# Kernel tuning notes

Hardware: AMD Instinct MI355X
Metric: run time of the kernel (lower is better)

Reference implementation:

```python
import jax, jax.numpy as jnp
import numpy as np

# Config (matches init_kwargs)
V = 32000      # vocab_size
H = 1024       # hidden_size
NH = 16        # num_heads
NKV = 4        # num_kv_heads
L = 4          # num_layers
FF = 4096      # intermediate_size
MAXPOS = 2048
HD = H // NH   # head_dim = 64
KVD = H * NKV // NH  # kv projection dim = 256
EPS = 1e-5


def setup_inputs() -> dict:
    key = jax.random.key(0)
    ks = iter(jax.random.split(key, 64))
    B, T = 1, 2048
    std = 0.02

    def w(shape):
        return jax.random.normal(next(ks), shape, dtype=jnp.float32) * std

    inp = {
        "input_ids": jax.random.randint(next(ks), (B, T), 0, V),
        "attention_mask": jnp.zeros((B, T), dtype=jnp.float32),
        "tok_emb": w((V, H)),
        "pos_emb": w((MAXPOS, H)),
        # stacked per-layer params; Linear weights stored as [in, out]
        "qW": w((L, H, H)),   "qb": jnp.zeros((L, H)),
        "kW": w((L, H, KVD)), "kb": jnp.zeros((L, KVD)),
        "vW": w((L, H, KVD)), "vb": jnp.zeros((L, KVD)),
        "oW": w((L, H, H)),   "ob": jnp.zeros((L, H)),
        "m1W": w((L, H, FF)), "m1b": jnp.zeros((L, FF)),
        "m2W": w((L, FF, H)), "m2b": jnp.zeros((L, H)),
        "ln1g": jnp.ones((L, H)), "ln1b": jnp.zeros((L, H)),
        "ln2g": jnp.ones((L, H)), "ln2b": jnp.zeros((L, H)),
        "lnfg": jnp.ones((H,)),   "lnfb": jnp.zeros((H,)),
        "headW": w((H, V)),  # head: Linear(H, V, bias=False), stored [in,out]
    }
    return inp


def _layer_norm(x, g, b):
    m = jnp.mean(x, axis=-1, keepdims=True)
    v = jnp.mean(jnp.square(x - m), axis=-1, keepdims=True)
    return (x - m) * jax.lax.rsqrt(v + EPS) * g + b


def _gqa_attn(x, mask, qW, qb, kW, kb, vW, vb, oW, ob):
    B, T, _ = x.shape
    G = NH // NKV  # query groups per kv head
    q = (x @ qW + qb).reshape(B, T, NH, HD).transpose(0, 2, 1, 3)        # [B,NH,T,HD]
    q = q.reshape(B, NKV, G, T, HD)                                      # [B,NKV,G,T,HD]
    k = (x @ kW + kb).reshape(B, T, NKV, HD).transpose(0, 2, 1, 3)       # [B,NKV,T,HD]
    v = (x @ vW + vb).reshape(B, T, NKV, HD).transpose(0, 2, 1, 3)       # [B,NKV,T,HD]
    # naive full score tensor [B,NKV,G,T,T] (as in the original module)
    scores = jnp.einsum("bkgqd,bksd->bkgqs", q, k) / jnp.sqrt(jnp.float32(HD))
    scores = scores + mask[:, None, None, None, :]  # additive mask over keys
    attn = jax.nn.softmax(scores, axis=-1)
    out = jnp.einsum("bkgqs,bksd->bkgqd", attn, v)                       # [B,NKV,G,T,HD]
    out = out.reshape(B, NH, T, HD).transpose(0, 2, 1, 3).reshape(B, T, H)
    return out @ oW + ob


def reference(input_ids, attention_mask, tok_emb, pos_emb,
              qW, qb, kW, kb, vW, vb, oW, ob,
              m1W, m1b, m2W, m2b,
              ln1g, ln1b, ln2g, ln2b, lnfg, lnfb, headW):
    B, T = input_ids.shape
    x = tok_emb[input_ids] + pos_emb[jnp.arange(T)][None, :, :]  # [B,T,H]
    for i in range(L):
        h = _layer_norm(x, ln1g[i], ln1b[i])
        x = x + _gqa_attn(h, attention_mask, qW[i], qb[i], kW[i], kb[i],
                          vW[i], vb[i], oW[i], ob[i])
        h = _layer_norm(x, ln2g[i], ln2b[i])
        h = jax.nn.gelu(h @ m1W[i] + m1b[i], approximate=False) @ m2W[i] + m2b[i]
        x = x + h
    x = _layer_norm(x, lnfg, lnfb)
    logits = x @ headW  # [B,T,V]
    return logits
```

## Files before the change

kernel.cpp:

```cpp
#include <hip/hip_runtime.h>
#include <stdint.h>
#include <math.h>

typedef __attribute__((ext_vector_type(8))) short bf16x8;
typedef __attribute__((ext_vector_type(4))) short bf16x4;
typedef __attribute__((ext_vector_type(4))) float f32x4;

__device__ __forceinline__ short f2bf(float f) {
  unsigned u = __builtin_bit_cast(unsigned, f);
  unsigned r = u + 0x7fffu + ((u >> 16) & 1u);
  return (short)(r >> 16);
}

__device__ __forceinline__ f32x4 mfma16(bf16x8 a, bf16x8 b, f32x4 c) {
  return __builtin_amdgcn_mfma_f32_16x16x32_bf16(a, b, c, 0, 0, 0);
}

__device__ __forceinline__ void gload16(const void* g, void* l) {
  __builtin_amdgcn_global_load_lds((const __attribute__((address_space(1))) void*)g,
                                   (__attribute__((address_space(3))) void*)l, 16, 0, 0);
}

__device__ __forceinline__ int swz(int row, int col) {
  return row * 64 + (((col >> 3) ^ (row & 7)) << 3) + (col & 7);
}

__global__ __launch_bounds__(256) void embed_k(const int* __restrict__ ids,
                                               const float* __restrict__ tok,
                                               const float* __restrict__ pos,
                                               float* __restrict__ x) {
  const int t = threadIdx.x, w = t >> 6, lane = t & 63;
  const int row = blockIdx.x * 4 + w;
  const int id = ids[row];
#pragma unroll
  for (int i = 0; i < 4; ++i) {
    const int c = (i * 64 + lane) * 4;
    const float4 a = *reinterpret_cast<const float4*>(tok + (size_t)id * 1024 + c);
    const float4 b = *reinterpret_cast<const float4*>(pos + (size_t)row * 1024 + c);
    float4 o = make_float4(a.x + b.x, a.y + b.y, a.z + b.z, a.w + b.w);
    *reinterpret_cast<float4*>(x + (size_t)row * 1024 + c) = o;
  }
}

__global__ __launch_bounds__(256) void ln_k(const float* __restrict__ x,
                                            const float* __restrict__ gw,
                                            const float* __restrict__ bw,
                                            short* __restrict__ out) {
  const int t = threadIdx.x, w = t >> 6, lane = t & 63;
  const int row = blockIdx.x * 4 + w;
  float4 v[4];
  float s = 0.f, q = 0.f;
#pragma unroll
  for (int i = 0; i < 4; ++i) {
    v[i] = *reinterpret_cast<const float4*>(x + (size_t)row * 1024 + (i * 64 + lane) * 4);
    s += v[i].x + v[i].y + v[i].z + v[i].w;
    q += v[i].x * v[i].x + v[i].y * v[i].y + v[i].z * v[i].z + v[i].w * v[i].w;
  }
#pragma unroll
  for (int o = 32; o > 0; o >>= 1) { s += __shfl_xor(s, o); q += __shfl_xor(q, o); }
  const float mean = s * (1.f / 1024.f);
  const float var  = q * (1.f / 1024.f) - mean * mean;
  const float rstd = rsqrtf(var + 1e-5f);
#pragma unroll
  for (int i = 0; i < 4; ++i) {
    const int c = (i * 64 + lane) * 4;
    const float4 gv = *reinterpret_cast<const float4*>(gw + c);
    const float4 bv = *reinterpret_cast<const float4*>(bw + c);
    bf16x4 ov = { f2bf((v[i].x - mean) * rstd * gv.x + bv.x),
                  f2bf((v[i].y - mean) * rstd * gv.y + bv.y),
                  f2bf((v[i].z - mean) * rstd * gv.z + bv.z),
                  f2bf((v[i].w - mean) * rstd * gv.w + bv.w) };
    *reinterpret_cast<bf16x4*>(out + (size_t)row * 1024 + c) = ov;
  }
}

__global__ __launch_bounds__(256) void tcvt_k(const float* __restrict__ W,
                                              short* __restrict__ Wt,
                                              int N, size_t inStride, size_t outStride,
                                              int rowOff, int ldOut, float scale) {
  __shared__ float T[128][68];
  const float* Win = W + blockIdx.z * inStride;
  short* Wout = Wt + blockIdx.z * outStride;
  const int n0 = blockIdx.x * 64, k0 = blockIdx.y * 128;
  const int t = threadIdx.x;
  const int nc = (t & 15) * 4, kr = t >> 4;
#pragma unroll
  for (int p = 0; p < 8; ++p) {
    const float4 v = *reinterpret_cast<const float4*>(Win + (size_t)(k0 + kr + 16 * p) * N + n0 + nc);
    T[kr + 16 * p][nc + 0] = v.x;
    T[kr + 16 * p][nc + 1] = v.y;
    T[kr + 16 * p][nc + 2] = v.z;
    T[kr + 16 * p][nc + 3] = v.w;
  }
  __syncthreads();
  const int n = t >> 2, ks = (t & 3) * 32;
  short tmp[32];
#pragma unroll
  for (int i = 0; i < 32; ++i) tmp[i] = f2bf(T[ks + i][n] * scale);
  short* op = Wout + (size_t)(rowOff + n0 + n) * ldOut + k0 + ks;
#pragma unroll
  for (int c = 0; c < 4; ++c)
    *reinterpret_cast<bf16x8*>(op + c * 8) = *reinterpret_cast<bf16x8*>(tmp + c * 8);
}

__global__ __launch_bounds__(256) void bqkv_k(const float* __restrict__ qb,
                                              const float* __restrict__ kb,
                                              const float* __restrict__ vb,
                                              float* __restrict__ o) {
  int l = blockIdx.y;
  int c = blockIdx.x * 256 + threadIdx.x;
  float v;
  if (c < 1024) v = qb[l * 1024 + c] * 0.125f;
  else if (c < 1280) v = kb[l * 256 + c - 1024];
  else v = vb[l * 256 + c - 1280];
  o[l * 1536 + c] = v;
}

__global__ __launch_bounds__(256) void vtr_k(const short* __restrict__ v, int vld,
                                             short* __restrict__ vt) {
  __shared__ short T[64][80];
  const int kvh = blockIdx.y;
  const int s0 = blockIdx.x * 64;
  const int t = threadIdx.x;
  const int row = t >> 3, ch = t & 7;
#pragma unroll
  for (int p = 0; p < 2; ++p) {
    int s = row + 32 * p;
    bf16x8 vv = *reinterpret_cast<const bf16x8*>(v + (size_t)(s0 + s) * vld + kvh * 64 + ch * 8);
    *reinterpret_cast<bf16x8*>(&T[s][ch * 8]) = vv;
  }
  __syncthreads();
#pragma unroll
  for (int p = 0; p < 2; ++p) {
    int d = row + 32 * p;
    short tmp[8];
#pragma unroll
    for (int i = 0; i < 8; ++i) tmp[i] = T[ch * 8 + i][d];
    *reinterpret_cast<bf16x8*>(vt + (size_t)(kvh * 64 + d) * 2048 + s0 + ch * 8) =
        *reinterpret_cast<bf16x8*>(tmp);
  }
}

template <int EPI, int XSWZ, int TILE>
__global__ __launch_bounds__(256, 4)
void gemm_bt(const short* __restrict__ A, const short* __restrict__ Wt,
             const float* __restrict__ bias, const float* __restrict__ resid,
             void* __restrict__ out, int M, int N, int K, int nbOff,
             short* __restrict__ vt) {
  constexpr int BN   = (TILE == 0) ? 128 : 64;
  constexpr int WN   = (TILE == 0) ? 64 : 32;
  constexpr int NT   = (TILE == 0) ? 4 : 2;
  constexpr int BISS = (TILE == 0) ? 4 : 2;
  __shared__ short As[128 * 64];
  __shared__ short Bs[BN * 64];
  const int t = threadIdx.x;
  const int lane = t & 63, w = t >> 6;
  const int g = lane >> 4, r = lane & 15;
  const int wr = w >> 1, wc = w & 1;

  int bx = blockIdx.x, by = blockIdx.y;
  if (XSWZ == 1) {
    const int nbx = gridDim.x, nby = gridDim.y, nwg = nbx * nby;
    const int bid = by * nbx + bx;
    const int q = nwg >> 3, rr = nwg & 7;
    const int xcd = bid & 7, loc = bid >> 3;
    const int sw = (xcd < rr ? xcd * (q + 1) : rr * (q + 1) + (xcd - rr) * q) + loc;
    by = sw % nby; bx = sw / nby;
  }
  const int m0 = by * 128, n0 = (bx + nbOff) * BN;

  f32x4 acc[4][NT];
#pragma unroll
  for (int i = 0; i < 4; ++i)
#pragma unroll
    for (int j = 0; j < NT; ++j) { f32x4 z = {0.f, 0.f, 0.f, 0.f}; acc[i][j] = z; }

  const int srow = lane >> 3, sslot = lane & 7;

  for (int k0 = 0; k0 < K; k0 += 64) {
#pragma unroll
    for (int i = 0; i < 4; ++i) {
      const int rowA = w * 32 + i * 8 + srow;
      const int colA = (sslot ^ (srow & 7)) << 3;
      gload16(A + (size_t)(m0 + rowA) * K + k0 + colA, &As[(w * 32 + i * 8) * 64]);
    }
#pragma unroll
    for (int i = 0; i < BISS; ++i) {
      const int rowB = w * (8 * BISS) + i * 8 + srow;
      const int colB = (sslot ^ (srow & 7)) << 3;
      gload16(Wt + (size_t)(n0 + rowB) * K + k0 + colB, &Bs[(w * (8 * BISS) + i * 8) * 64]);
    }
    __syncthreads();
#pragma unroll
    for (int kk = 0; kk < 64; kk += 32) {
      bf16x8 af[4], bfg[NT];
#pragma unroll
      for (int mt = 0; mt < 4; ++mt)
        af[mt] = *reinterpret_cast<const bf16x8*>(&As[swz(wr * 64 + mt * 16 + r, kk + g * 8)]);
#pragma unroll
      for (int nt = 0; nt < NT; ++nt)
        bfg[nt] = *reinterpret_cast<const bf16x8*>(&Bs[swz(wc * WN + nt * 16 + r, kk + g * 8)]);
#pragma unroll
      for (int mt = 0; mt < 4; ++mt)
#pragma unroll
        for (int nt = 0; nt < NT; ++nt)
          acc[mt][nt] = mfma16(af[mt], bfg[nt], acc[mt][nt]);
    }
    __syncthreads();
  }
#pragma unroll
  for (int nt = 0; nt < NT; ++nt) {
    const int col = n0 + wc * WN + nt * 16 + r;
    const float bv = (EPI == 3) ? 0.f : bias[col];
#pragma unroll
    for (int mt = 0; mt < 4; ++mt) {
      const int rowb = m0 + wr * 64 + mt * 16 + 4 * g;
      short vs[4];
#pragma unroll
      for (int j = 0; j < 4; ++j) {
        const int row = rowb + j;
        const size_t oi = (size_t)row * N + col;
        float vv = acc[mt][nt][j] + bv;
        if (EPI == 0) {
          ((short*)out)[oi] = f2bf(vv);
        } else if (EPI == 1) {
          vv = 0.5f * vv * (1.f + erff(vv * 0.70710678118654752f));
          ((short*)out)[oi] = f2bf(vv);
        } else if (EPI == 2) {
          ((float*)out)[oi] = resid[oi] + vv;
        } else if (EPI == 3) {
          ((float*)out)[oi] = vv;
        } else {
          short bb = f2bf(vv);
          ((short*)out)[oi] = bb;
          vs[j] = bb;
        }
      }
      if (EPI == 4 && col >= 1280) {
        bf16x4 pk = { vs[0], vs[1], vs[2], vs[3] };
        *reinterpret_cast<bf16x4*>(vt + (size_t)(col - 1280) * 2048 + rowb) = pk;
      }
    }
  }
}

template <int EPI>
__global__ __launch_bounds__(256)
void gemm_k(const short* __restrict__ A, const float* __restrict__ W,
            const float* __restrict__ bias, const float* resid, void* out,
            int M, int N, int K, float scale) {
  __shared__ short As[128 * 64];
  __shared__ short Bs[128 * 64];
  const int t = threadIdx.x;
  const int lane = t & 63;
  const int g = lane >> 4, r = lane & 15;
  const int wid = t >> 6, wr = wid >> 1, wc = wid & 1;
  const int m0 = blockIdx.y * 128, n0 = blockIdx.x * 128;
  f32x4 acc[4][4];
#pragma unroll
  for (int i = 0; i < 4; ++i)
#pragma unroll
    for (int j = 0; j < 4; ++j) { f32x4 z = {0.f, 0.f, 0.f, 0.f}; acc[i][j] = z; }
  const int arow = t >> 3, ac = t & 7;
  const int bnn = t >> 1, bkh = t & 1;
  for (int k0 = 0; k0 < K; k0 += 64) {
#pragma unroll
    for (int p = 0; p < 4; ++p) {
      int row = arow + 32 * p;
      bf16x8 av = *reinterpret_cast<const bf16x8*>(A + (size_t)(m0 + row) * K + k0 + ac * 8);
      *reinterpret_cast<bf16x8*>(&As[swz(row, ac * 8)]) = av;
    }
#pragma unroll
    for (int p = 0; p < 8; ++p) {
      int kg = 4 * (bkh + 2 * p);
      const float* wp = W + (size_t)(k0 + kg) * N + n0 + bnn;
      bf16x4 wv = { f2bf(wp[0]), f2bf(wp[(size_t)N]), f2bf(wp[(size_t)2 * N]), f2bf(wp[(size_t)3 * N]) };
      *reinterpret_cast<bf16x4*>(&Bs[swz(bnn, kg)]) = wv;
    }
    __syncthreads();
#pragma unroll
    for (int kk = 0; kk < 64; kk += 32) {
      bf16x8 af[4], bfg[4];
#pragma unroll
      for (int mt = 0; mt < 4; ++mt)
        af[mt] = *reinterpret_cast<const bf16x8*>(&As[swz(wr * 64 + mt * 16 + r, kk + g * 8)]);
#pragma unroll
      for (int nt = 0; nt < 4; ++nt)
        bfg[nt] = *reinterpret_cast<const bf16x8*>(&Bs[swz(wc * 64 + nt * 16 + r, kk + g * 8)]);
#pragma unroll
      for (int mt = 0; mt < 4; ++mt)
#pragma unroll
        for (int nt = 0; nt < 4; ++nt)
          acc[mt][nt] = mfma16(af[mt], bfg[nt], acc[mt][nt]);
    }
    __syncthreads();
  }
#pragma unroll
  for (int nt = 0; nt < 4; ++nt) {
    const int col = n0 + wc * 64 + nt * 16 + r;
    const float bv = (EPI == 3) ? 0.f : bias[col];
#pragma unroll
    for (int mt = 0; mt < 4; ++mt) {
#pragma unroll
      for (int j = 0; j < 4; ++j) {
        const int row = m0 + wr * 64 + mt * 16 + 4 * g + j;
        const size_t oi = (size_t)row * N + col;
        float vv = acc[mt][nt][j] + bv;
        if (EPI == 0) {
          ((short*)out)[oi] = f2bf(vv * scale);
        } else if (EPI == 1) {
          vv = 0.5f * vv * (1.f + erff(vv * 0.70710678118654752f));
          ((short*)out)[oi] = f2bf(vv);
        } else if (EPI == 2) {
          ((float*)out)[oi] = resid[oi] + vv;
        } else {
          ((float*)out)[oi] = vv;
        }
      }
    }
  }
}

__global__ __launch_bounds__(256) void attn_k(const short* __restrict__ q, int qld,
                                              const short* __restrict__ k, int kld,
                                              const short* __restrict__ vt,
                                              const float* __restrict__ mask,
                                              short* __restrict__ o) {
  __shared__ short Ks[2][64 * 64];
  __shared__ short Vs[2][64 * 64];
  const int t = threadIdx.x, lane = t & 63, w = t >> 6;
  const int g = lane >> 4, r = lane & 15;
  const int h = blockIdx.y, qb = blockIdx.x, kvh = h >> 2;
  const int qrow = qb * 64 + w * 16 + r;

  const short* qp = q + (size_t)qrow * qld + h * 64;
  bf16x8 qf0 = *reinterpret_cast<const bf16x8*>(qp + g * 8);
  bf16x8 qf1 = *reinterpret_cast<const bf16x8*>(qp + 32 + g * 8);

  const short* kbase = k + kvh * 64;
  const short* vbase = vt + (size_t)kvh * 64 * 2048;

  f32x4 oacc[4];
#pragma unroll
  for (int i = 0; i < 4; ++i) { f32x4 z = {0.f, 0.f, 0.f, 0.f}; oacc[i] = z; }
  float m_run = -INFINITY, l_run = 0.f;

  const int srow = w * 8 + (lane >> 3), schunk = lane & 7;

#pragma unroll
  for (int p = 0; p < 2; ++p) {
    const int rr = srow + 32 * p;
    const int cc = (schunk ^ (rr & 7)) << 3;
    gload16(kbase + (size_t)rr * kld + cc, (char*)Ks + p * 4096 + w * 1024);
    gload16(vbase + (size_t)rr * 2048 + cc, (char*)Vs + p * 4096 + w * 1024);
  }
  asm volatile("s_waitcnt vmcnt(0)" ::: "memory");
  __syncthreads();

  for (int it = 0; it < 32; ++it) {
    const int cur = it & 1;
    if (it < 31) {
      const int s1 = (it + 1) * 64;
#pragma unroll
      for (int p = 0; p < 2; ++p) {
        const int rr = srow + 32 * p;
        const int cc = (schunk ^ (rr & 7)) << 3;
        gload16(kbase + (size_t)(s1 + rr) * kld + cc,
                (char*)Ks + (cur ^ 1) * 8192 + p * 4096 + w * 1024);
        gload16(vbase + (size_t)rr * 2048 + s1 + cc,
                (char*)Vs + (cur ^ 1) * 8192 + p * 4096 + w * 1024);
      }
    }
    const int s0 = it * 64;
    const short* Kc = Ks[cur];
    const short* Vc = Vs[cur];

    f32x4 sa[4];
#pragma unroll
    for (int st = 0; st < 4; ++st) {
      bf16x8 kf0 = *reinterpret_cast<const bf16x8*>(&Kc[swz(st * 16 + r, g * 8)]);
      bf16x8 kf1 = *reinterpret_cast<const bf16x8*>(&Kc[swz(st * 16 + r, 32 + g * 8)]);
      f32x4 z = {0.f, 0.f, 0.f, 0.f};
      z = mfma16(kf0, qf0, z);
      z = mfma16(kf1, qf1, z);
      sa[st] = z;
    }
    float sv[16];
    float pmax = -INFINITY;
#pragma unroll
    for (int st = 0; st < 4; ++st) {
      const float4 mv = *reinterpret_cast<const float4*>(mask + s0 + st * 16 + 4 * g);
#pragma unroll
      for (int j = 0; j < 4; ++j) {
        float xx = sa[st][j] + ((const float*)&mv)[j];
        sv[st * 4 + j] = xx;
        pmax = fmaxf(pmax, xx);
      }
    }
    pmax = fmaxf(pmax, __shfl_xor(pmax, 16));
    pmax = fmaxf(pmax, __shfl_xor(pmax, 32));
    float m_new = fmaxf(m_run, pmax);
    float corr = __expf(m_run - m_new);
    float psum = 0.f;
    short pb[16];
#pragma unroll
    for (int i = 0; i < 16; ++i) {
      float p = __expf(sv[i] - m_new);
      psum += p;
      pb[i] = f2bf(p);
    }
    psum += __shfl_xor(psum, 16);
    psum += __shfl_xor(psum, 32);
    l_run = l_run * corr + psum;
    m_run = m_new;
#pragma unroll
    for (int dt = 0; dt < 4; ++dt)
#pragma unroll
      for (int j = 0; j < 4; ++j) oacc[dt][j] *= corr;

#pragma unroll
    for (int hs = 0; hs < 2; ++hs) {
      bf16x8 pf = { pb[hs * 8 + 0], pb[hs * 8 + 1], pb[hs * 8 + 2], pb[hs * 8 + 3],
                    pb[hs * 8 + 4], pb[hs * 8 + 5], pb[hs * 8 + 6], pb[hs * 8 + 7] };
#pragma unroll
      for (int dt = 0; dt < 4; ++dt) {
        int d = dt * 16 + r;
        int c1 = 4 * g + 32 * hs;
        bf16x4 va  = *reinterpret_cast<const bf16x4*>(&Vc[swz(d, c1)]);
        bf16x4 vb2 = *reinterpret_cast<const bf16x4*>(&Vc[swz(d, c1 + 16)]);
        bf16x8 vf = { va[0], va[1], va[2], va[3], vb2[0], vb2[1], vb2[2], vb2[3] };
        oacc[dt] = mfma16(vf, pf, oacc[dt]);
      }
    }
    asm volatile("s_waitcnt vmcnt(0)" ::: "memory");
    __syncthreads();
  }
  float inv = 1.f / l_run;
#pragma unroll
  for (int dt = 0; dt < 4; ++dt) {
    bf16x4 ov = { f2bf(oacc[dt][0] * inv), f2bf(oacc[dt][1] * inv),
                  f2bf(oacc[dt][2] * inv), f2bf(oacc[dt][3] * inv) };
    *reinterpret_cast<bf16x4*>(o + (size_t)qrow * 1024 + h * 64 + dt * 16 + 4 * g) = ov;
  }
}

extern "C" void kernel_launch(void* const* d_in, const int* in_sizes, int n_in,
                              void* d_out, int out_size, void* d_ws, size_t ws_size,
                              hipStream_t stream) {
  const int*   ids   = (const int*)d_in[0];
  const float* mask  = (const float*)d_in[1];
  const float* tok   = (const float*)d_in[2];
  const float* pos   = (const float*)d_in[3];
  const float* qW    = (const float*)d_in[4];
  const float* qbias = (const float*)d_in[5];
  const float* kW    = (const float*)d_in[6];
  const float* kbias = (const float*)d_in[7];
  const float* vW    = (const float*)d_in[8];
  const float* vbias = (const float*)d_in[9];
  const float* oW    = (const float*)d_in[10];
  const float* obias = (const float*)d_in[11];
  const float* m1W   = (const float*)d_in[12];
  const float* m1b   = (const float*)d_in[13];
  const float* m2W   = (const float*)d_in[14];
  const float* m2b   = (const float*)d_in[15];
  const float* ln1g  = (const float*)d_in[16];
  const float* ln1b  = (const float*)d_in[17];
  const float* ln2g  = (const float*)d_in[18];
  const float* ln2b  = (const float*)d_in[19];
  const float* lnfg  = (const float*)d_in[20];
  const float* lnfb  = (const float*)d_in[21];
  const float* headW = (const float*)d_in[22];
  float* out = (float*)d_out;

  char* ws = (char*)d_ws;
  float* x   = (float*)ws;
  short* xb  = (short*)(ws + 8388608ull);

  const size_t OFF_QKV  = 12582912ull;
  const size_t OFF_AO   = 18874368ull;
  const size_t OFF_FF   = 23068672ull;
  const size_t OFF_BQ   = 39845888ull;
  const size_t OFF_WQKV = 39870464ull;
  const size_t OFF_WO   = 52453376ull;
  const size_t OFF_WM1  = 60841984ull;
  const size_t OFF_WM2  = 94396416ull;
  const size_t OFF_WH   = 127950848ull;
  const size_t NEED     = 193486848ull;

  if (ws_size >= NEED) {
    short* qkv  = (short*)(ws + OFF_QKV);
    short* ao   = (short*)(ws + OFF_AO);
    short* ff   = (short*)(ws + OFF_FF);
    short* vt   = ff;
    float* bqv  = (float*)(ws + OFF_BQ);
    short* Wqkv = (short*)(ws + OFF_WQKV);
    short* Wo   = (short*)(ws + OFF_WO);
    short* Wm1  = (short*)(ws + OFF_WM1);
    short* Wm2  = (short*)(ws + OFF_WM2);
    short* Wh   = (short*)(ws + OFF_WH);

    tcvt_k<<<dim3(16, 8, 4), 256, 0, stream>>>(qW, Wqkv, 1024, 1048576ull, 1572864ull, 0, 1024, 0.125f);
    tcvt_k<<<dim3(4, 8, 4),  256, 0, stream>>>(kW, Wqkv, 256,  262144ull,  1572864ull, 1024, 1024, 1.f);
    tcvt_k<<<dim3(4, 8, 4),  256, 0, stream>>>(vW, Wqkv, 256,  262144ull,  1572864ull, 1280, 1024, 1.f);
    tcvt_k<<<dim3(16, 8, 4), 256, 0, stream>>>(oW, Wo, 1024, 1048576ull, 1048576ull, 0, 1024, 1.f);
    tcvt_k<<<dim3(64, 8, 4), 256, 0, stream>>>(m1W, Wm1, 4096, 4194304ull, 4194304ull, 0, 1024, 1.f);
    tcvt_k<<<dim3(16, 32, 4), 256, 0, stream>>>(m2W, Wm2, 1024, 4194304ull, 4194304ull, 0, 4096, 1.f);
    tcvt_k<<<dim3(500, 8, 1), 256, 0, stream>>>(headW, Wh, 32000, 0ull, 0ull, 0, 1024, 1.f);
    bqkv_k<<<dim3(6, 4), 256, 0, stream>>>(qbias, kbias, vbias, bqv);

    embed_k<<<512, 256, 0, stream>>>(ids, tok, pos, x);

    for (int l = 0; l < 4; ++l) {
      short* Wq_l  = Wqkv + (size_t)l * 1536 * 1024;
      short* Wo_l  = Wo   + (size_t)l * 1024 * 1024;
      short* Wm1_l = Wm1  + (size_t)l * 4096 * 1024;
      short* Wm2_l = Wm2  + (size_t)l * 1024 * 4096;

      ln_k<<<512, 256, 0, stream>>>(x, ln1g + l * 1024, ln1b + l * 1024, xb);
      gemm_bt<4, 0, 1><<<dim3(24, 16), 256, 0, stream>>>(xb, Wq_l, bqv + l * 1536, nullptr,
                                                         qkv, 2048, 1536, 1024, 0, vt);
      attn_k<<<dim3(32, 16), 256, 0, stream>>>(qkv, 1536, qkv + 1024, 1536, vt, mask, ao);
      gemm_bt<2, 0, 1><<<dim3(16, 16), 256, 0, stream>>>(ao, Wo_l, obias + l * 1024, x,
                                                         x, 2048, 1024, 1024, 0, nullptr);
      ln_k<<<512, 256, 0, stream>>>(x, ln2g + l * 1024, ln2b + l * 1024, xb);
      gemm_bt<1, 1, 1><<<dim3(64, 16), 256, 0, stream>>>(xb, Wm1_l, m1b + l * 4096, nullptr,
                                                         ff, 2048, 4096, 1024, 0, nullptr);
      gemm_bt<2, 1, 1><<<dim3(16, 16), 256, 0, stream>>>(ff, Wm2_l, m2b + l * 1024, x,
                                                         x, 2048, 1024, 4096, 0, nullptr);
    }
    ln_k<<<512, 256, 0, stream>>>(x, lnfg, lnfb, xb);
    gemm_bt<3, 1, 0><<<dim3(125, 16), 256, 0, stream>>>(xb, Wh, nullptr, nullptr,
                                                        out, 2048, 32000, 1024, 0, nullptr);
    gemm_bt<3, 1, 0><<<dim3(125, 16), 256, 0, stream>>>(xb, Wh, nullptr, nullptr,
                                                        out, 2048, 32000, 1024, 125, nullptr);
  } else {
    short* qbf = (short*)(ws + (12u << 20));
    short* kbf = (short*)(ws + (16u << 20));
    short* vbf = (short*)(ws + (17u << 20));
    short* ao  = (short*)(ws + (18u << 20));
    short* ff  = (short*)(ws + (22u << 20));
    short* vtf = (short*)(ws + (38u << 20));

    embed_k<<<512, 256, 0, stream>>>(ids, tok, pos, x);
    for (int l = 0; l < 4; ++l) {
      ln_k<<<512, 256, 0, stream>>>(x, ln1g + l * 1024, ln1b + l * 1024, xb);
      gemm_k<0><<<dim3(8, 16), 256, 0, stream>>>(xb, qW + (size_t)l * 1024 * 1024,
          qbias + l * 1024, nullptr, qbf, 2048, 1024, 1024, 0.125f);
      gemm_k<0><<<dim3(2, 16), 256, 0, stream>>>(xb, kW + (size_t)l * 1024 * 256,
          kbias + l * 256, nullptr, kbf, 2048, 256, 1024, 1.f);
      gemm_k<0><<<dim3(2, 16), 256, 0, stream>>>(xb, vW + (size_t)l * 1024 * 256,
          vbias + l * 256, nullptr, vbf, 2048, 256, 1024, 1.f);
      vtr_k<<<dim3(32, 4), 256, 0, stream>>>(vbf, 256, vtf);
      attn_k<<<dim3(32, 16), 256, 0, stream>>>(qbf, 1024, kbf, 256, vtf, mask, ao);
      gemm_k<2><<<dim3(8, 16), 256, 0, stream>>>(ao, oW + (size_t)l * 1024 * 1024,
          obias + l * 1024, x, x, 2048, 1024, 1024, 1.f);
      ln_k<<<512, 256, 0, stream>>>(x, ln2g + l * 1024, ln2b + l * 1024, xb);
      gemm_k<1><<<dim3(32, 16), 256, 0, stream>>>(xb, m1W + (size_t)l * 1024 * 4096,
          m1b + l * 4096, nullptr, ff, 2048, 4096, 1024, 1.f);
      gemm_k<2><<<dim3(8, 16), 256, 0, stream>>>(ff, m2W + (size_t)l * 4096 * 1024,
          m2b + l * 1024, x, x, 2048, 1024, 4096, 1.f);
    }
    ln_k<<<512, 256, 0, stream>>>(x, lnfg, lnfb, xb);
    gemm_k<3><<<dim3(250, 16), 256, 0, stream>>>(xb, headW, nullptr, nullptr, out,
        2048, 32000, 1024, 1.f);
  }
}
```

Baseline: 1.176 ms.

## Add 256x256 double-buffered LM-head GEMM kernel with XCD-aware block remap

```diff
diff --git a/kernel.cpp b/kernel.cpp
--- a/kernel.cpp
+++ b/kernel.cpp
@@ -138,6 +138,112 @@
     for (int i = 0; i < 8; ++i) tmp[i] = T[ch * 8 + i][d];
     *reinterpret_cast<bf16x8*>(vt + (size_t)(kvh * 64 + d) * 2048 + s0 + ch * 8) =
         *reinterpret_cast<bf16x8*>(tmp);
+  }
+}
+
+__global__ __launch_bounds__(512, 2)
+void gemm_h8(const short* __restrict__ A, const short* __restrict__ Wt,
+             float* __restrict__ out, int M, int N, int K) {
+  __shared__ short As[2][256 * 64];
+  __shared__ short Bs[2][256 * 64];
+  const int t = threadIdx.x;
+  const int lane = t & 63, w = t >> 6;
+  const int g = lane >> 4, r = lane & 15;
+  const int wm = w >> 2, wn = w & 3;
+
+  int bx = blockIdx.x, by = blockIdx.y;
+  {
+    const int nbx = gridDim.x, nby = gridDim.y, nwg = nbx * nby;
+    const int bid = by * nbx + bx;
+    const int q = nwg >> 3, rr = nwg & 7;
+    const int xcd = bid & 7, loc = bid >> 3;
+    const int sw = (xcd < rr ? xcd * (q + 1) : rr * (q + 1) + (xcd - rr) * q) + loc;
+    by = sw % nby; bx = sw / nby;
+  }
+  const int m0 = by * 256, n0 = bx * 256;
+
+  f32x4 acc[8][4];
+#pragma unroll
+  for (int i = 0; i < 8; ++i)
+#pragma unroll
+    for (int j = 0; j < 4; ++j) { f32x4 z = {0.f, 0.f, 0.f, 0.f}; acc[i][j] = z; }
+
+  const int srow8 = lane >> 3, sslot = lane & 7;
+  const int NTILES = K >> 6;
+
+#pragma unroll
+  for (int rnd = 0; rnd < 4; ++rnd) {
+    const int row = rnd * 64 + w * 8 + srow8;
+    const int col = (sslot ^ (row & 7)) << 3;
+    gload16(A + (size_t)(m0 + row) * K + col, &As[0][(rnd * 64 + w * 8) * 64]);
+    gload16(Wt + (size_t)(n0 + row) * K + col, &Bs[0][(rnd * 64 + w * 8) * 64]);
+  }
+  asm volatile("s_waitcnt vmcnt(0)" ::: "memory");
+  __builtin_amdgcn_s_barrier();
+  __builtin_amdgcn_sched_barrier(0);
+
+  for (int tt = 0; tt < NTILES; ++tt) {
+    const int cur = tt & 1;
+    const short* Ac = As[cur];
+    const short* Bc = Bs[cur];
+    short* An = &As[cur ^ 1][0];
+    short* Bn = &Bs[cur ^ 1][0];
+    const bool pref = (tt + 1 < NTILES);
+    const int k1 = (tt + 1) << 6;
+
+#pragma unroll
+    for (int q = 0; q < 4; ++q) {
+      const int qm = q >> 1, qn = q & 1;
+      if (q < 2 && pref) {
+#pragma unroll
+        for (int h = 0; h < 2; ++h) {
+          const int rnd = 2 * q + h;
+          const int row = rnd * 64 + w * 8 + srow8;
+          const int col = (sslot ^ (row & 7)) << 3;
+          gload16(A + (size_t)(m0 + row) * K + k1 + col, &An[(rnd * 64 + w * 8) * 64]);
+          gload16(Wt + (size_t)(n0 + row) * K + k1 + col, &Bn[(rnd * 64 + w * 8) * 64]);
+        }
+      }
+      bf16x8 af[2][4], bfr[2][2];
+#pragma unroll
+      for (int kk = 0; kk < 2; ++kk) {
+#pragma unroll
+        for (int mt = 0; mt < 4; ++mt)
+          af[kk][mt] = *reinterpret_cast<const bf16x8*>(
+              &Ac[swz(wm * 128 + qm * 64 + mt * 16 + r, kk * 32 + g * 8)]);
+#pragma unroll
+        for (int nt = 0; nt < 2; ++nt)
+          bfr[kk][nt] = *reinterpret_cast<const bf16x8*>(
+              &Bc[swz(wn * 64 + qn * 32 + nt * 16 + r, kk * 32 + g * 8)]);
+      }
+      __builtin_amdgcn_s_barrier();
+      __builtin_amdgcn_s_setprio(1);
+#pragma unroll
+      for (int kk = 0; kk < 2; ++kk)
+#pragma unroll
+        for (int mt = 0; mt < 4; ++mt)
+#pragma unroll
+          for (int nt = 0; nt < 2; ++nt)
+            acc[qm * 4 + mt][qn * 2 + nt] =
+                mfma16(af[kk][mt], bfr[kk][nt], acc[qm * 4 + mt][qn * 2 + nt]);
+      __builtin_amdgcn_s_setprio(0);
+      if (q == 3) {
+        asm volatile("s_waitcnt vmcnt(0)" ::: "memory");
+      }
+      __builtin_amdgcn_s_barrier();
+      if (q == 3) __builtin_amdgcn_sched_barrier(0);
+    }
+  }
+#pragma unroll
+  for (int mi = 0; mi < 8; ++mi) {
+    const int row = m0 + wm * 128 + mi * 16 + 4 * g;
+#pragma unroll
+    for (int ni = 0; ni < 4; ++ni) {
+      const int col = n0 + wn * 64 + ni * 16 + r;
+#pragma unroll
+      for (int j = 0; j < 4; ++j)
+        out[(size_t)(row + j) * N + col] = acc[mi][ni][j];
+    }
   }
 }
 
@@ -529,10 +635,7 @@
                                                          x, 2048, 1024, 4096, 0, nullptr);
     }
     ln_k<<<512, 256, 0, stream>>>(x, lnfg, lnfb, xb);
-    gemm_bt<3, 1, 0><<<dim3(125, 16), 256, 0, stream>>>(xb, Wh, nullptr, nullptr,
-                                                        out, 2048, 32000, 1024, 0, nullptr);
-    gemm_bt<3, 1, 0><<<dim3(125, 16), 256, 0, stream>>>(xb, Wh, nullptr, nullptr,
-                                                        out, 2048, 32000, 1024, 125, nullptr);
+    gemm_h8<<<dim3(125, 8), 512, 0, stream>>>(xb, Wh, out, 2048, 32000, 1024);
   } else {
     short* qbf = (short*)(ws + (12u << 20));
     short* kbf = (short*)(ws + (16u << 20));
```

New measurement: 1.250 ms. +6.3%, slower.
